# Performance work log

Hardware: AMD Instinct MI355X
Metric: run time of the kernel (lower is better)

Reference implementation:

```python
import jax, jax.numpy as jnp
import numpy as np

FEAT, HW, C, M, U, B = 2048, 14, 20, 64, 128, 4


def _grid_sample_one(img, grid):
    # img: [M, H, W]; grid: [H, W, 2] normalized coords (x, y), align_corners=True, zero padding
    H, W = img.shape[-2], img.shape[-1]
    gx = (grid[..., 0] + 1.0) * 0.5 * (W - 1)
    gy = (grid[..., 1] + 1.0) * 0.5 * (H - 1)
    x0 = jnp.floor(gx).astype(jnp.int32); x1 = x0 + 1
    y0 = jnp.floor(gy).astype(jnp.int32); y1 = y0 + 1

    def gather(yi, xi):
        valid = (yi >= 0) & (yi < H) & (xi >= 0) & (xi < W)
        yc = jnp.clip(yi, 0, H - 1); xc = jnp.clip(xi, 0, W - 1)
        return img[:, yc, xc] * valid.astype(img.dtype)  # [M, H, W]

    w00 = (x1 - gx) * (y1 - gy); w01 = (gx - x0) * (y1 - gy)
    w10 = (x1 - gx) * (gy - y0); w11 = (gx - x0) * (gy - y0)
    return (gather(y0, x0) * w00 + gather(y0, x1) * w01 +
            gather(y1, x0) * w10 + gather(y1, x1) * w11)


def setup_inputs() -> dict:
    key = jax.random.key(0)
    ks = jax.random.split(key, 5)
    x = jax.random.normal(ks[0], (B, FEAT, HW, HW), jnp.float32)
    W_parcel = jax.random.normal(ks[1], (C, M, FEAT), jnp.float32) * 0.02
    W_stn = jax.random.normal(ks[2], (C, 6, M * (HW // 2) ** 2), jnp.float32) * 1e-3
    b_stn = jnp.tile(jnp.array([1.0, 0.0, 0.0, 0.0, 1.0, 0.0], jnp.float32), (C, 1))
    Wg = jax.random.normal(ks[3], (C, C - 1, U, 2 * M), jnp.float32) * 0.02
    w_phi = jax.random.normal(ks[4], (1, U), jnp.float32) * 0.05
    b_phi = jnp.zeros((1,), jnp.float32)
    return {"x": x, "W_parcel": W_parcel, "W_stn": W_stn, "b_stn": b_stn,
            "Wg": Wg, "w_phi": w_phi, "b_phi": b_phi}


def reference(x, W_parcel, W_stn, b_stn, Wg, w_phi, b_phi):
    b, _, H, W = x.shape
    # per-class 1x1 conv parcels: [B, C, M, H, W]
    x_tmp = jnp.einsum('bfhw,cmf->bcmhw', x, W_parcel)
    # relu + 2x2 maxpool -> [B, C, M, 7, 7]
    pooled = jax.nn.relu(x_tmp).reshape(b, C, M, H // 2, 2, W // 2, 2).max(axis=(4, 6))
    flat = pooled.reshape(b, C, M * (H // 2) * (W // 2))
    theta = (jnp.einsum('bck,cjk->bcj', flat, W_stn) + b_stn).reshape(b, C, 2, 3)
    # affine grid (align_corners=True): base[h, w] = [x_norm, y_norm, 1]
    xs = jnp.linspace(-1.0, 1.0, W); ys = jnp.linspace(-1.0, 1.0, H)
    base = jnp.stack(jnp.broadcast_arrays(xs[None, :], ys[:, None], jnp.ones((H, W))), -1)
    grid = jnp.einsum('bcij,hwj->bchwi', theta, base)  # [B, C, H, W, 2]
    # STN sampling of the pre-relu parcel maps
    x_obj = jax.vmap(jax.vmap(_grid_sample_one))(x_tmp, grid)  # [B, C, M, H, W]
    # pairwise relation: relu(Wa[i,j] x_obj[i] + Wb[i,j] x_obj[j]) summed over j != i
    jidx = jnp.asarray(np.array([[k for k in range(C) if k != c] for c in range(C)]))
    Wa, Wb = Wg[..., :M], Wg[..., M:]
    A = jnp.einsum('ckum,bcmhw->bckuhw', Wa, x_obj)
    Bp = jnp.einsum('ckum,bckmhw->bckuhw', Wb, x_obj[:, jidx])
    rel = jax.nn.relu(A + Bp).sum(axis=2)          # [B, C, U, H, W]
    rel_mean = rel.mean(axis=(-2, -1))             # [B, C, U]  (adaptive avg pool 1x1)
    out = jnp.einsum('bcu,ou->bco', rel_mean, w_phi)[..., 0] + b_phi  # [B, C]
    return out
```

## Files before the change

### kernel.cpp

```cpp
#include <hip/hip_runtime.h>

#define FEAT 2048
#define HWD 14
#define NPIX 196
#define C_CLS 20
#define M_DIM 64
#define U_DIM 128
#define B_SZ 4
#define K_REL 19
#define NPOOL 49

typedef __attribute__((ext_vector_type(8))) short bf16x8s;
typedef __attribute__((ext_vector_type(8))) unsigned short ushort8v;
typedef __attribute__((ext_vector_type(4))) float f32x4;
typedef __attribute__((ext_vector_type(4))) unsigned int uint4v;

__device__ inline unsigned short f2bf(float f) {
    unsigned u = __builtin_bit_cast(unsigned, f);
    unsigned r = (u + 0x7FFF + ((u >> 16) & 1)) >> 16;
    return (unsigned short)r;
}

__global__ __launch_bounds__(256) void prep_kernel(
        const float* __restrict__ x, const float* __restrict__ Wp,
        const float* __restrict__ Wg,
        unsigned short* __restrict__ xts, unsigned short* __restrict__ Awp,
        unsigned short* __restrict__ Awg) {
    __shared__ unsigned short SM[128 * 136];
    const int blk = blockIdx.x;
    const int tid = threadIdx.x;
    const int lane = tid & 63, wv = tid >> 6;
    const int l15 = lane & 15, lq = lane >> 4;

    if (blk < 128) {
        unsigned short (*T)[210] = (unsigned short (*)[210])SM;
        const int b = blk >> 5;
        const int s = blk & 31;
        const float* xb = x + ((size_t)b * FEAT + s * 64) * NPIX;
        for (int i = tid; i < 64 * NPIX; i += 256) {
            int kk = i / NPIX, hw = i - kk * NPIX;
            T[kk][hw] = f2bf(xb[(size_t)kk * NPIX + hw]);
        }
        __syncthreads();
        unsigned short* ob = xts + ((size_t)(b * 32 + s)) * 1664 * 8;
        for (int i = tid; i < 1664; i += 256) {
            int ch = i / 208, row = i - ch * 208;
            ushort8v o;
#pragma unroll
            for (int j = 0; j < 8; j++)
                o[j] = (row < NPIX) ? T[ch * 8 + j][row] : (unsigned short)0;
            *(ushort8v*)(ob + (size_t)i * 8) = o;
        }
    } else if (blk < 288) {
        unsigned short (*TP)[264] = (unsigned short (*)[264])SM;
        const int p = blk - 128;
        const int c = p >> 3, kc = p & 7;
        const float* wsrc = Wp + ((size_t)c * M_DIM) * FEAT + kc * 256;
#pragma unroll
        for (int it = 0; it < 16; it++) {
            int i4 = tid + it * 256;
            int m = i4 >> 6, c4 = i4 & 63;
            float4 v = *(const float4*)(wsrc + (size_t)m * FEAT + c4 * 4);
            TP[m][c4 * 4 + 0] = f2bf(v.x);
            TP[m][c4 * 4 + 1] = f2bf(v.y);
            TP[m][c4 * 4 + 2] = f2bf(v.z);
            TP[m][c4 * 4 + 3] = f2bf(v.w);
        }
        __syncthreads();
#pragma unroll
        for (int fr = 0; fr < 8; fr++) {
            int ss = wv;
            int fi = fr;
            int rt = fi >> 1, f = fi & 1;
            int m = rt * 16 + l15;
            int kl = ss * 64 + f * 32 + lq * 8;
            bf16x8s vfrag = *(const bf16x8s*)(&TP[m][kl]);
            int s = kc * 4 + ss;
            *(bf16x8s*)(Awp + (((size_t)(c * 32 + s) * 8 + fi) * 64 + lane) * 8) = vfrag;
        }
    } else {
        unsigned short (*TG)[136] = (unsigned short (*)[136])SM;
        const int ck = blk - 288;
        const float* gsrc = Wg + (size_t)ck * U_DIM * 128;
#pragma unroll
        for (int it = 0; it < 16; it++) {
            int i4 = tid + it * 256;
            int u = i4 >> 5, c4 = i4 & 31;
            float4 v = *(const float4*)(gsrc + (size_t)u * 128 + c4 * 4);
            TG[u][c4 * 4 + 0] = f2bf(v.x);
            TG[u][c4 * 4 + 1] = f2bf(v.y);
            TG[u][c4 * 4 + 2] = f2bf(v.z);
            TG[u][c4 * 4 + 3] = f2bf(v.w);
        }
        __syncthreads();
#pragma unroll
        for (int fr = 0; fr < 8; fr++) {
            int fi = fr;
            int ut = fi >> 2, ks = fi & 3;
            int u = wv * 32 + ut * 16 + l15;
            int mm = ks * 32 + lq * 8;
            bf16x8s vfrag = *(const bf16x8s*)(&TG[u][mm]);
            *(bf16x8s*)(Awg + (((size_t)(ck * 4 + wv) * 8 + fi) * 64 + lane) * 8) = vfrag;
        }
    }
}

__global__ __launch_bounds__(256) void gemm_kernel(
        const unsigned short* __restrict__ xts,
        const unsigned short* __restrict__ Awp,
        float* __restrict__ xsp) {
    const int c = blockIdx.x, b = blockIdx.y, ks = blockIdx.z;
    const int tid = threadIdx.x;
    const int lane = tid & 63, wv = tid >> 6;
    const int l15 = lane & 15, lq = lane >> 4;
    const int t0 = (wv == 0) ? 0 : (3 * wv + 1);
    const int nt = (wv == 0) ? 4 : 3;

    const unsigned short* xsrc = xts + (size_t)b * 32 * 1664 * 8;
    const unsigned short* asrc = Awp + (size_t)c * 256 * 64 * 8;
    const int s0 = ks * 8;

    bf16x8s A0[8], A1[8], B0[8], B1[8];
    auto aload = [&](int s, bf16x8s (&A)[8]) {
#pragma unroll
        for (int fi = 0; fi < 8; fi++)
            A[fi] = *(const bf16x8s*)(asrc + (((size_t)s * 8 + fi) * 64 + lane) * 8);
    };
    auto bload = [&](int s, bf16x8s (&B)[8]) {
#pragma unroll
        for (int q = 0; q < 4; q++) {
            if (q < nt) {
#pragma unroll
                for (int f = 0; f < 2; f++)
                    B[q * 2 + f] = *(const bf16x8s*)(xsrc +
                        ((size_t)s * 1664 + (f * 4 + lq) * 208 + (t0 + q) * 16 + l15) * 8);
            }
        }
    };

    f32x4 acc[4][4];
#pragma unroll
    for (int q = 0; q < 4; q++)
#pragma unroll
        for (int rt = 0; rt < 4; rt++) acc[q][rt] = (f32x4){0.f, 0.f, 0.f, 0.f};

    auto compute = [&](bf16x8s (&A)[8], bf16x8s (&B)[8]) {
#pragma unroll
        for (int q = 0; q < 4; q++) {
            if (q < nt) {
#pragma unroll
                for (int rt = 0; rt < 4; rt++)
#pragma unroll
                    for (int f = 0; f < 2; f++)
                        acc[q][rt] = __builtin_amdgcn_mfma_f32_16x16x32_bf16(
                            A[rt * 2 + f], B[q * 2 + f], acc[q][rt], 0, 0, 0);
            }
        }
    };

    aload(s0, A0); bload(s0, B0);
#pragma unroll
    for (int sp = 0; sp < 4; sp++) {
        aload(s0 + 2 * sp + 1, A1); bload(s0 + 2 * sp + 1, B1);
        compute(A0, B0);
        if (sp < 3) { aload(s0 + 2 * sp + 2, A0); bload(s0 + 2 * sp + 2, B0); }
        compute(A1, B1);
    }

    float* ob = xsp + ((size_t)(ks * B_SZ + b) * C_CLS + c) * 64 * 208;
#pragma unroll
    for (int q = 0; q < 4; q++) {
        if (q < nt) {
            int tt = t0 + q;
#pragma unroll
            for (int rt = 0; rt < 4; rt++)
#pragma unroll
                for (int r = 0; r < 4; r++)
                    ob[(rt * 16 + lq * 4 + r) * 208 + tt * 16 + l15] = acc[q][rt][r];
        }
    }
}

__global__ __launch_bounds__(512) void phases_kernel(
        const float* __restrict__ xsp,
        const float* __restrict__ Wstn,
        const float* __restrict__ bstn,
        unsigned short* __restrict__ x_objT) {
    __shared__ __align__(16) char smem[78336];
    float* xs     = (float*)smem;
    float* pooled = (float*)(smem + 53504);
    float* red    = (float*)(smem + 66048);

    const int c = blockIdx.x, b = blockIdx.y;
    const int tid = threadIdx.x;

    const size_t S = (size_t)B_SZ * C_CLS * 13312;
    const float* pb = xsp + (size_t)(b * C_CLS + c) * 13312;
#pragma unroll 2
    for (int it = 0; it < 26; it++) {
        int i = tid + it * 512;
        float v = pb[i] + pb[i + S] + pb[i + 2 * S] + pb[i + 3 * S];
        xs[(i / 208) * 209 + (i % 208)] = v;
    }
    __syncthreads();

    for (int i = tid; i < 3136; i += 512) {
        int m = i / NPOOL, p = i - m * NPOOL;
        int ph = p / 7, pw = p - ph * 7;
        const float* bp = &xs[m * 209 + ph * 2 * HWD + pw * 2];
        float v = fmaxf(fmaxf(bp[0], bp[1]), fmaxf(bp[HWD], bp[HWD + 1]));
        pooled[i] = fmaxf(v, 0.f);
    }
    __syncthreads();

    float sj[6] = {0, 0, 0, 0, 0, 0};
#pragma unroll
    for (int it = 0; it < 7; it++) {
        int kk = tid + it * 512;
        if (kk < 3136) {
            float f = pooled[kk];
#pragma unroll
            for (int j = 0; j < 6; j++)
                sj[j] += f * Wstn[((size_t)c * 6 + j) * 3136 + kk];
        }
    }
#pragma unroll
    for (int j = 0; j < 6; j++) red[j * 512 + tid] = sj[j];
    __syncthreads();
    for (int off = 256; off > 0; off >>= 1) {
        if (tid < off) {
#pragma unroll
            for (int j = 0; j < 6; j++)
                red[j * 512 + tid] += red[j * 512 + tid + off];
        }
        __syncthreads();
    }
    float th[6];
#pragma unroll
    for (int j = 0; j < 6; j++) th[j] = red[j * 512] + bstn[c * 6 + j];

    unsigned short* obase = x_objT + ((size_t)(b * C_CLS + c) * 208) * 64;
    for (int i = tid; i < 12 * 64; i += 512)
        obase[(size_t)(NPIX + i / 64) * 64 + (i & 63)] = 0;

    const int m = tid & 63;
    const int hwg = tid >> 6;
    unsigned short* ob = obase + m;
    const float* xrow = &xs[m * 209];
    for (int it = 0; it < 25; it++) {
        int hw = hwg + it * 8;
        if (hw >= NPIX) break;
        int h = hw / HWD, w = hw - h * HWD;
        float fx = -1.f + w * (2.f / 13.f);
        float fy = -1.f + h * (2.f / 13.f);
        float gxn = th[0] * fx + th[1] * fy + th[2];
        float gyn = th[3] * fx + th[4] * fy + th[5];
        float gx = (gxn + 1.f) * 0.5f * (HWD - 1);
        float gy = (gyn + 1.f) * 0.5f * (HWD - 1);
        float x0f = floorf(gx), y0f = floorf(gy);
        int x0 = (int)x0f, y0 = (int)y0f;
        int x1 = x0 + 1, y1 = y0 + 1;
        auto gat = [&](int yi, int xi) -> float {
            bool v = (yi >= 0) & (yi < HWD) & (xi >= 0) & (xi < HWD);
            int yc = min(max(yi, 0), HWD - 1);
            int xc = min(max(xi, 0), HWD - 1);
            return v ? xrow[yc * HWD + xc] : 0.f;
        };
        float xw1 = (float)x1 - gx, xw0 = gx - (float)x0;
        float yw1 = (float)y1 - gy, yw0 = gy - (float)y0;
        float val = gat(y0, x0) * xw1 * yw1 + gat(y0, x1) * xw0 * yw1 +
                    gat(y1, x0) * xw1 * yw0 + gat(y1, x1) * xw0 * yw0;
        ob[(size_t)hw * 64] = f2bf(val);
    }
}

#define MP 136
__global__ __launch_bounds__(256) void relation_mfma_kernel(
        const unsigned short* __restrict__ x_objT,
        const unsigned short* __restrict__ Awg,
        float* __restrict__ partial) {
    __shared__ unsigned short Xs[208 * MP];
    const int k = blockIdx.x;
    const int c = blockIdx.y;
    const int b = blockIdx.z;
    const int kj = (k < c) ? k : k + 1;
    const int tid = threadIdx.x;
    const int lane = tid & 63;
    const int wv = tid >> 6;
    const int l15 = lane & 15;
    const int lq = lane >> 4;

    bf16x8s AF[2][4];
    const unsigned short* ab = Awg + (((size_t)(c * K_REL + k) * 4 + wv) * 8 * 64) * 8;
#pragma unroll
    for (int ut = 0; ut < 2; ut++)
#pragma unroll
        for (int ks = 0; ks < 4; ks++)
            AF[ut][ks] = *(const bf16x8s*)(ab + ((size_t)(ut * 4 + ks) * 64 + lane) * 8);

    const unsigned short* xc = x_objT + ((size_t)(b * C_CLS + c)) * 208 * 64;
    const unsigned short* xk = x_objT + ((size_t)(b * C_CLS + kj)) * 208 * 64;
#pragma unroll
    for (int it = 0; it < 13; it++) {
        int i = tid + it * 256;
        int hw = i >> 4, ch = i & 15;
        const unsigned short* src = (ch < 8 ? xc : xk) + (size_t)hw * 64 + (ch & 7) * 8;
        *(uint4v*)(&Xs[hw * MP + ch * 8]) = *(const uint4v*)src;
    }
    __syncthreads();

    float csum[2][4];
#pragma unroll
    for (int ut = 0; ut < 2; ut++)
#pragma unroll
        for (int r = 0; r < 4; r++) csum[ut][r] = 0.f;

    for (int t = 0; t < 13; t++) {
        bf16x8s BF[4];
#pragma unroll
        for (int ks = 0; ks < 4; ks++)
            BF[ks] = *(const bf16x8s*)(&Xs[(t * 16 + l15) * MP + ks * 32 + lq * 8]);
        f32x4 acc0 = {0.f, 0.f, 0.f, 0.f}, acc1 = {0.f, 0.f, 0.f, 0.f};
#pragma unroll
        for (int ks = 0; ks < 4; ks++) {
            acc0 = __builtin_amdgcn_mfma_f32_16x16x32_bf16(AF[0][ks], BF[ks], acc0, 0, 0, 0);
            acc1 = __builtin_amdgcn_mfma_f32_16x16x32_bf16(AF[1][ks], BF[ks], acc1, 0, 0, 0);
        }
#pragma unroll
        for (int r = 0; r < 4; r++) {
            csum[0][r] += fmaxf(acc0[r], 0.f);
            csum[1][r] += fmaxf(acc1[r], 0.f);
        }
    }
#pragma unroll
    for (int mask = 1; mask < 16; mask <<= 1) {
#pragma unroll
        for (int ut = 0; ut < 2; ut++)
#pragma unroll
            for (int r = 0; r < 4; r++)
                csum[ut][r] += __shfl_xor(csum[ut][r], mask, 64);
    }
    if (l15 == 0) {
        float* pp = partial + (((size_t)b * C_CLS + c) * K_REL + k) * U_DIM;
#pragma unroll
        for (int ut = 0; ut < 2; ut++)
#pragma unroll
            for (int r = 0; r < 4; r++)
                pp[wv * 32 + ut * 16 + lq * 4 + r] = csum[ut][r];
    }
}

__global__ __launch_bounds__(128) void final_kernel(
        const float* __restrict__ partial, const float* __restrict__ wphi,
        const float* __restrict__ bphi, float* __restrict__ out) {
    int bc = blockIdx.x;
    int u = threadIdx.x;
    float s = 0.f;
    for (int k = 0; k < K_REL; k++)
        s += partial[((size_t)bc * K_REL + k) * U_DIM + u];
    s *= wphi[u];
    __shared__ float red[128];
    red[u] = s;
    __syncthreads();
    for (int off = 64; off > 0; off >>= 1) {
        if (u < off) red[u] += red[u + off];
        __syncthreads();
    }
    if (u == 0) out[bc] = red[0] / (float)NPIX + bphi[0];
}

extern "C" void kernel_launch(void* const* d_in, const int* in_sizes, int n_in,
                              void* d_out, int out_size, void* d_ws, size_t ws_size,
                              hipStream_t stream) {
    const float* x    = (const float*)d_in[0];
    const float* Wp   = (const float*)d_in[1];
    const float* Wstn = (const float*)d_in[2];
    const float* bstn = (const float*)d_in[3];
    const float* Wg   = (const float*)d_in[4];
    const float* wphi = (const float*)d_in[5];
    const float* bphi = (const float*)d_in[6];
    float* out = (float*)d_out;
    char* wsb = (char*)d_ws;

    unsigned short* xts    = (unsigned short*)(wsb);
    unsigned short* Awp    = (unsigned short*)(wsb + 3407872);
    unsigned short* Awg    = (unsigned short*)(wsb + 8650752);
    float* xsp             = (float*)(wsb + 21102592);
    unsigned short* x_objT = (unsigned short*)(wsb + 38141952);
    float* partial         = (float*)(wsb + 40271872);

    prep_kernel<<<668, 256, 0, stream>>>(x, Wp, Wg, xts, Awp, Awg);
    gemm_kernel<<<dim3(C_CLS, B_SZ, 4), 256, 0, stream>>>(xts, Awp, xsp);
    phases_kernel<<<dim3(C_CLS, B_SZ), 512, 0, stream>>>(xsp, Wstn, bstn, x_objT);
    relation_mfma_kernel<<<dim3(K_REL, C_CLS, B_SZ), 256, 0, stream>>>(x_objT, Awg, partial);
    final_kernel<<<80, 128, 0, stream>>>(partial, wphi, bphi, out);
}
```

Measured before the change: 66.08 us.

## Fuse parcel GEMM into phases kernel with in-block split-K reduction in LDS

Merges the split-K parcel GEMM into the phases kernel. Each block now runs the GEMM with 8 waves split into two K halves, and the two halves are reduced in shared memory instead of writing four fp32 partial slices to global memory and reading them back. This removes one kernel launch and the global round trip of the partial sums. In exchange, the GEMM grid shrinks from 320 blocks to 80, and each wave walks twice as many K steps, which cuts parallelism for the GEMM phase.

```diff
diff --git a/kernel.cpp b/kernel.cpp
--- a/kernel.cpp
+++ b/kernel.cpp
@@ -105,84 +105,9 @@
     }
 }
 
-__global__ __launch_bounds__(256) void gemm_kernel(
+__global__ __launch_bounds__(512) void gemmphase_kernel(
         const unsigned short* __restrict__ xts,
         const unsigned short* __restrict__ Awp,
-        float* __restrict__ xsp) {
-    const int c = blockIdx.x, b = blockIdx.y, ks = blockIdx.z;
-    const int tid = threadIdx.x;
-    const int lane = tid & 63, wv = tid >> 6;
-    const int l15 = lane & 15, lq = lane >> 4;
-    const int t0 = (wv == 0) ? 0 : (3 * wv + 1);
-    const int nt = (wv == 0) ? 4 : 3;
-
-    const unsigned short* xsrc = xts + (size_t)b * 32 * 1664 * 8;
-    const unsigned short* asrc = Awp + (size_t)c * 256 * 64 * 8;
-    const int s0 = ks * 8;
-
-    bf16x8s A0[8], A1[8], B0[8], B1[8];
-    auto aload = [&](int s, bf16x8s (&A)[8]) {
-#pragma unroll
-        for (int fi = 0; fi < 8; fi++)
-            A[fi] = *(const bf16x8s*)(asrc + (((size_t)s * 8 + fi) * 64 + lane) * 8);
-    };
-    auto bload = [&](int s, bf16x8s (&B)[8]) {
-#pragma unroll
-        for (int q = 0; q < 4; q++) {
-            if (q < nt) {
-#pragma unroll
-                for (int f = 0; f < 2; f++)
-                    B[q * 2 + f] = *(const bf16x8s*)(xsrc +
-                        ((size_t)s * 1664 + (f * 4 + lq) * 208 + (t0 + q) * 16 + l15) * 8);
-            }
-        }
-    };
-
-    f32x4 acc[4][4];
-#pragma unroll
-    for (int q = 0; q < 4; q++)
-#pragma unroll
-        for (int rt = 0; rt < 4; rt++) acc[q][rt] = (f32x4){0.f, 0.f, 0.f, 0.f};
-
-    auto compute = [&](bf16x8s (&A)[8], bf16x8s (&B)[8]) {
-#pragma unroll
-        for (int q = 0; q < 4; q++) {
-            if (q < nt) {
-#pragma unroll
-                for (int rt = 0; rt < 4; rt++)
-#pragma unroll
-                    for (int f = 0; f < 2; f++)
-                        acc[q][rt] = __builtin_amdgcn_mfma_f32_16x16x32_bf16(
-                            A[rt * 2 + f], B[q * 2 + f], acc[q][rt], 0, 0, 0);
-            }
-        }
-    };
-
-    aload(s0, A0); bload(s0, B0);
-#pragma unroll
-    for (int sp = 0; sp < 4; sp++) {
-        aload(s0 + 2 * sp + 1, A1); bload(s0 + 2 * sp + 1, B1);
-        compute(A0, B0);
-        if (sp < 3) { aload(s0 + 2 * sp + 2, A0); bload(s0 + 2 * sp + 2, B0); }
-        compute(A1, B1);
-    }
-
-    float* ob = xsp + ((size_t)(ks * B_SZ + b) * C_CLS + c) * 64 * 208;
-#pragma unroll
-    for (int q = 0; q < 4; q++) {
-        if (q < nt) {
-            int tt = t0 + q;
-#pragma unroll
-            for (int rt = 0; rt < 4; rt++)
-#pragma unroll
-                for (int r = 0; r < 4; r++)
-                    ob[(rt * 16 + lq * 4 + r) * 208 + tt * 16 + l15] = acc[q][rt][r];
-        }
-    }
-}
-
-__global__ __launch_bounds__(512) void phases_kernel(
-        const float* __restrict__ xsp,
         const float* __restrict__ Wstn,
         const float* __restrict__ bstn,
         unsigned short* __restrict__ x_objT) {
@@ -193,14 +118,90 @@
 
     const int c = blockIdx.x, b = blockIdx.y;
     const int tid = threadIdx.x;
-
-    const size_t S = (size_t)B_SZ * C_CLS * 13312;
-    const float* pb = xsp + (size_t)(b * C_CLS + c) * 13312;
-#pragma unroll 2
-    for (int it = 0; it < 26; it++) {
-        int i = tid + it * 512;
-        float v = pb[i] + pb[i + S] + pb[i + 2 * S] + pb[i + 3 * S];
-        xs[(i / 208) * 209 + (i % 208)] = v;
+    const int lane = tid & 63, wv = tid >> 6;
+    const int l15 = lane & 15, lq = lane >> 4;
+    const int kh = wv >> 2;
+    const int cg = wv & 3;
+    const int t0 = (cg == 0) ? 0 : (3 * cg + 1);
+    const int nt = (cg == 0) ? 4 : 3;
+
+    const unsigned short* xsrc = xts + (size_t)b * 32 * 1664 * 8;
+    const unsigned short* asrc = Awp + (size_t)c * 256 * 64 * 8;
+    const int s0 = kh * 16;
+
+    bf16x8s A0[8], A1[8], B0[8], B1[8];
+    auto aload = [&](int s, bf16x8s (&A)[8]) {
+#pragma unroll
+        for (int fi = 0; fi < 8; fi++)
+            A[fi] = *(const bf16x8s*)(asrc + (((size_t)s * 8 + fi) * 64 + lane) * 8);
+    };
+    auto bload = [&](int s, bf16x8s (&B)[8]) {
+#pragma unroll
+        for (int q = 0; q < 4; q++) {
+            if (q < nt) {
+#pragma unroll
+                for (int f = 0; f < 2; f++)
+                    B[q * 2 + f] = *(const bf16x8s*)(xsrc +
+                        ((size_t)s * 1664 + (f * 4 + lq) * 208 + (t0 + q) * 16 + l15) * 8);
+            }
+        }
+    };
+
+    f32x4 acc[4][4];
+#pragma unroll
+    for (int q = 0; q < 4; q++)
+#pragma unroll
+        for (int rt = 0; rt < 4; rt++) acc[q][rt] = (f32x4){0.f, 0.f, 0.f, 0.f};
+
+    auto compute = [&](bf16x8s (&A)[8], bf16x8s (&B)[8]) {
+#pragma unroll
+        for (int q = 0; q < 4; q++) {
+            if (q < nt) {
+#pragma unroll
+                for (int rt = 0; rt < 4; rt++)
+#pragma unroll
+                    for (int f = 0; f < 2; f++)
+                        acc[q][rt] = __builtin_amdgcn_mfma_f32_16x16x32_bf16(
+                            A[rt * 2 + f], B[q * 2 + f], acc[q][rt], 0, 0, 0);
+            }
+        }
+    };
+
+    aload(s0, A0); bload(s0, B0);
+#pragma unroll
+    for (int sp = 0; sp < 8; sp++) {
+        aload(s0 + 2 * sp + 1, A1); bload(s0 + 2 * sp + 1, B1);
+        compute(A0, B0);
+        if (sp < 7) { aload(s0 + 2 * sp + 2, A0); bload(s0 + 2 * sp + 2, B0); }
+        compute(A1, B1);
+    }
+
+    if (kh == 0) {
+#pragma unroll
+        for (int q = 0; q < 4; q++) {
+            if (q < nt) {
+                int tt = t0 + q;
+#pragma unroll
+                for (int rt = 0; rt < 4; rt++)
+#pragma unroll
+                    for (int r = 0; r < 4; r++)
+                        xs[(rt * 16 + lq * 4 + r) * 209 + tt * 16 + l15] = acc[q][rt][r];
+            }
+        }
+    }
+    __syncthreads();
+    if (kh == 1) {
+#pragma unroll
+        for (int q = 0; q < 4; q++) {
+            if (q < nt) {
+                int tt = t0 + q;
+#pragma unroll
+                for (int rt = 0; rt < 4; rt++)
+#pragma unroll
+                    for (int r = 0; r < 4; r++)
+                        xs[(rt * 16 + lq * 4 + r) * 209 + tt * 16 + l15] += acc[q][rt][r];
+            }
+        }
     }
     __syncthreads();
 
@@ -385,13 +386,11 @@
     unsigned short* xts    = (unsigned short*)(wsb);
     unsigned short* Awp    = (unsigned short*)(wsb + 3407872);
     unsigned short* Awg    = (unsigned short*)(wsb + 8650752);
-    float* xsp             = (float*)(wsb + 21102592);
-    unsigned short* x_objT = (unsigned short*)(wsb + 38141952);
-    float* partial         = (float*)(wsb + 40271872);
+    unsigned short* x_objT = (unsigned short*)(wsb + 21102592);
+    float* partial         = (float*)(wsb + 23232512);
 
     prep_kernel<<<668, 256, 0, stream>>>(x, Wp, Wg, xts, Awp, Awg);
-    gemm_kernel<<<dim3(C_CLS, B_SZ, 4), 256, 0, stream>>>(xts, Awp, xsp);
-    phases_kernel<<<dim3(C_CLS, B_SZ), 512, 0, stream>>>(xsp, Wstn, bstn, x_objT);
+    gemmphase_kernel<<<dim3(C_CLS, B_SZ), 512, 0, stream>>>(xts, Awp, Wstn, bstn, x_objT);
     relation_mfma_kernel<<<dim3(K_REL, C_CLS, B_SZ), 256, 0, stream>>>(x_objT, Awg, partial);
     final_kernel<<<80, 128, 0, stream>>>(partial, wphi, bphi, out);
 }
```

After: 65.02 us, median of 2. Within noise of the previous version (-1.6%).
